# Kernel optimization log

Hardware: AMD Instinct MI355X
Metric: run time of the kernel (lower is better)

## Reference

```python
import jax, jax.numpy as jnp
import numpy as np

N_HEADS = 16
N_EMBD = 1024
HEAD_DIM = N_EMBD // N_HEADS
WINDOW = 512
B, T = 2, 2048


def setup_inputs() -> dict:
    key = jax.random.key(0)
    ks = jax.random.split(key, 5)
    s = 0.02
    return {
        "x": jax.random.normal(ks[0], (B, T, N_EMBD), dtype=jnp.float32),
        "Wq": jax.random.normal(ks[1], (N_EMBD, N_EMBD), dtype=jnp.float32) * s,
        "Wk": jax.random.normal(ks[2], (N_EMBD, N_EMBD), dtype=jnp.float32) * s,
        "Wv": jax.random.normal(ks[3], (N_EMBD, N_EMBD), dtype=jnp.float32) * s,
        "Wo": jax.random.normal(ks[4], (N_EMBD, N_EMBD), dtype=jnp.float32) * s,
    }


def _sliding_window_mask(T, window):
    # mask[i, j] True iff max(0, i-window+1) <= j <= i  (causal banded)
    i = jnp.arange(T)[:, None]
    j = jnp.arange(T)[None, :]
    return (j <= i) & (j > i - window)


def reference(x, Wq, Wk, Wv, Wo):
    Bb, Tt, C = x.shape
    # nn.Linear applies x @ W.T; we store W as [in, out] so just x @ W
    def heads(w):
        return (x @ w).reshape(Bb, Tt, N_HEADS, HEAD_DIM).transpose(0, 2, 1, 3)
    q, k, v = heads(Wq), heads(Wk), heads(Wv)  # [B, H, T, D]
    scores = jnp.einsum("bhqd,bhkd->bhqk", q, k) / jnp.sqrt(jnp.float32(HEAD_DIM))
    mask = _sliding_window_mask(Tt, WINDOW)  # [T, T]
    scores = jnp.where(mask[None, None], scores, jnp.float32(-jnp.inf))
    attn = jax.nn.softmax(scores, axis=-1)
    out = jnp.einsum("bhqk,bhkd->bhqd", attn, v)  # [B, H, T, D]
    out = out.transpose(0, 2, 1, 3).reshape(Bb, Tt, C)
    return out @ Wo
```

## Files before the change

### kernel.cpp

```cpp
#include <hip/hip_runtime.h>

#define B_SZ 2
#define T_SZ 2048
#define C_SZ 1024
#define K_SZ 1024
#define QKV_LD 3072
#define H_CNT 16
#define D_SZ 64
#define WIN 512

typedef __bf16 bf16_t;
typedef bf16_t bf16x8 __attribute__((ext_vector_type(8)));
typedef bf16_t bf16x4 __attribute__((ext_vector_type(4)));
typedef float f32x4 __attribute__((ext_vector_type(4)));
typedef unsigned int u32;

__device__ __forceinline__ f32x4 mfma16(bf16x8 a, bf16x8 b, f32x4 c) {
  return __builtin_amdgcn_mfma_f32_16x16x32_bf16(a, b, c, 0, 0, 0);
}

__device__ __forceinline__ void gload_lds16(const void* gsrc, void* ldst) {
  auto g = (__attribute__((address_space(1))) void*)(unsigned long long)gsrc;
  auto l = (__attribute__((address_space(3))) void*)(unsigned int)(unsigned long long)ldst;
  __builtin_amdgcn_global_load_lds(g, l, 16, 0, 0);
}

__global__ __launch_bounds__(256) void prep(
    const float* __restrict__ x, bf16_t* __restrict__ xb,
    const float* __restrict__ W0, const float* __restrict__ W1,
    const float* __restrict__ W2, const float* __restrict__ W3,
    bf16_t* __restrict__ T0, bf16_t* __restrict__ T1,
    bf16_t* __restrict__ T2, bf16_t* __restrict__ T3) {
  if (blockIdx.z == 4) {
    const int base = (blockIdx.y * 32 + blockIdx.x) * 256 + threadIdx.x;
#pragma unroll
    for (int j = 0; j < 4; ++j) {
      const int idx = base + j * 262144;
      const float4 v = ((const float4*)x)[idx];
      bf16x4 r;
      r[0] = (bf16_t)v.x; r[1] = (bf16_t)v.y; r[2] = (bf16_t)v.z; r[3] = (bf16_t)v.w;
      ((bf16x4*)xb)[idx] = r;
    }
    return;
  }
  __shared__ float tile[32][33];
  const float* W = blockIdx.z == 0 ? W0 : blockIdx.z == 1 ? W1 : blockIdx.z == 2 ? W2 : W3;
  bf16_t* Tt = blockIdx.z == 0 ? T0 : blockIdx.z == 1 ? T1 : blockIdx.z == 2 ? T2 : T3;
  const int tx = threadIdx.x & 31, ty = threadIdx.x >> 5;
  const int r0 = blockIdx.y * 32, c0 = blockIdx.x * 32;
#pragma unroll
  for (int i = 0; i < 4; ++i)
    tile[ty + i * 8][tx] = W[(size_t)(r0 + ty + i * 8) * C_SZ + c0 + tx];
  __syncthreads();
#pragma unroll
  for (int i = 0; i < 4; ++i)
    Tt[(size_t)(c0 + ty + i * 8) * C_SZ + r0 + tx] = (bf16_t)tile[tx][ty + i * 8];
}

#define GM_NT 16

__global__ __launch_bounds__(512, 2) void gemm256(
    const bf16_t* __restrict__ A, const bf16_t* __restrict__ Bt,
    bf16_t* __restrict__ C, bf16_t* __restrict__ Vt) {
  __shared__ __align__(16) bf16_t As[2][256 * 64];
  __shared__ __align__(16) bf16_t Bs[2][192 * 64];
  const int wg = blockIdx.x + 16 * blockIdx.y;
  const int swz = (wg & 7) * 32 + (wg >> 3);
  const int bx = swz & 15, by = swz >> 4;
  const int m0 = by * 256, n0 = bx * 192;
  const int tid = threadIdx.x, w = tid >> 6, lane = tid & 63;
  const int wr = w >> 1, wc = w & 1;
  const int g = lane >> 4, l15 = lane & 15, sw = l15 & 7;
  const int srow = lane >> 3, sj = lane & 7;

  f32x4 acc[4][6] = {};

  auto stageA = [&](int buf, int half, int k0) {
#pragma unroll
    for (int q8 = 0; q8 < 2; ++q8) {
      const int rg = w * 16 + q8 * 8;
      gload_lds16(A + (size_t)(m0 + half * 128 + rg + srow) * K_SZ + k0 + ((sj ^ srow) << 3),
                  &As[buf][half * 8192 + rg * 64]);
    }
  };
  auto stageB = [&](int buf, int third, int k0) {
    const int rg = third * 64 + w * 8;
    gload_lds16(Bt + (size_t)(n0 + rg + srow) * K_SZ + k0 + ((sj ^ srow) << 3),
                &Bs[buf][rg * 64]);
  };

  stageA(0, 0, 0); stageA(0, 1, 0);
  stageB(0, 0, 0); stageB(0, 1, 0); stageB(0, 2, 0);

#define LDAF(MF, KK) \
  (*(const bf16x8*)&As[buf][(wr * 64 + (MF) * 16 + l15) * 64 + \
                            ((((KK) << 2) | g) ^ sw) * 8])
#define LDBF(NF, KK) \
  (*(const bf16x8*)&Bs[buf][(wc * 96 + (NF) * 16 + l15) * 64 + \
                            ((((KK) << 2) | g) ^ sw) * 8])
#define MROW(MF, AF)                              \
  acc[(MF)][0] = mfma16(AF, b0, acc[(MF)][0]);    \
  acc[(MF)][1] = mfma16(AF, b1, acc[(MF)][1]);    \
  acc[(MF)][2] = mfma16(AF, b2, acc[(MF)][2]);    \
  acc[(MF)][3] = mfma16(AF, b3, acc[(MF)][3]);    \
  acc[(MF)][4] = mfma16(AF, b4, acc[(MF)][4]);    \
  acc[(MF)][5] = mfma16(AF, b5, acc[(MF)][5]);

#pragma unroll 2
  for (int t = 0; t < GM_NT; ++t) {
    const int buf = t & 1, nb = buf ^ 1;
    const int k1 = (t + 1) * 64;
    asm volatile("s_waitcnt vmcnt(0)" ::: "memory");
    __builtin_amdgcn_s_barrier();

    {
      bf16x8 a0 = LDAF(0, 0), a1 = LDAF(1, 0), a2 = LDAF(2, 0), a3 = LDAF(3, 0);
      bf16x8 b0 = LDBF(0, 0), b1 = LDBF(1, 0), b2 = LDBF(2, 0),
             b3 = LDBF(3, 0), b4 = LDBF(4, 0), b5 = LDBF(5, 0);
      if (t < GM_NT - 1) { stageA(nb, 0, k1); stageA(nb, 1, k1); }
      __builtin_amdgcn_s_barrier();
      __builtin_amdgcn_s_setprio(1);
      MROW(0, a0) MROW(1, a1) MROW(2, a2) MROW(3, a3)
      __builtin_amdgcn_s_setprio(0);
      __builtin_amdgcn_s_barrier();
    }
    {
      bf16x8 a0 = LDAF(0, 1), a1 = LDAF(1, 1), a2 = LDAF(2, 1), a3 = LDAF(3, 1);
      bf16x8 b0 = LDBF(0, 1), b1 = LDBF(1, 1), b2 = LDBF(2, 1),
             b3 = LDBF(3, 1), b4 = LDBF(4, 1), b5 = LDBF(5, 1);
      if (t < GM_NT - 1) { stageB(nb, 0, k1); stageB(nb, 1, k1); stageB(nb, 2, k1); }
      __builtin_amdgcn_s_barrier();
      __builtin_amdgcn_s_setprio(1);
      MROW(0, a0) MROW(1, a1) MROW(2, a2) MROW(3, a3)
      __builtin_amdgcn_s_setprio(0);
    }
  }

#pragma unroll
  for (int mf = 0; mf < 4; ++mf) {
    const int row = m0 + wr * 64 + mf * 16 + g * 4;
#pragma unroll
    for (int nf = 0; nf < 6; ++nf) {
      const int colb = n0 + wc * 96 + nf * 16;
      if (colb >= 2048) {
        const int d = colb - 2048 + l15;
        const size_t vo =
            ((size_t)((row >> 11) * 16 + (d >> 6)) * 64 + (d & 63)) * (size_t)T_SZ +
            (row & (T_SZ - 1));
        union { bf16_t h4[4]; uint2 u; } pk;
#pragma unroll
        for (int i = 0; i < 4; ++i) pk.h4[i] = (bf16_t)acc[mf][nf][i];
        *(uint2*)(Vt + vo) = pk.u;
      } else {
#pragma unroll
        for (int i = 0; i < 4; ++i)
          C[(size_t)(row + i) * QKV_LD + colb + l15] = (bf16_t)acc[mf][nf][i];
      }
    }
  }
}

__global__ __launch_bounds__(512, 4) void gemm128(
    const bf16_t* __restrict__ A, int lda, const bf16_t* __restrict__ Bt,
    float* __restrict__ C, int N) {
  __shared__ __align__(16) bf16_t As[2][128 * 64];
  __shared__ __align__(16) bf16_t Bs[2][128 * 64];
  const int wg = blockIdx.x + 8 * blockIdx.y;
  const int swz = (wg & 7) * 32 + (wg >> 3);
  const int bx = swz & 7, by = swz >> 3;
  const int m0 = by * 128, n0 = bx * 128;
  const int tid = threadIdx.x, w = tid >> 6, lane = tid & 63;
  const int wr = w >> 2, wc = w & 3;
  const int g = lane >> 4, l15 = lane & 15, sw = l15 & 7;
  const int srow = lane >> 3, sj = lane & 7;

  f32x4 acc[4][2] = {};

  auto stage = [&](int buf, int k0) {
#pragma unroll
    for (int half = 0; half < 2; ++half) {
      const int rg = half * 64 + w * 8;
      gload_lds16(A + (size_t)(m0 + rg + srow) * lda + k0 + ((sj ^ srow) << 3),
                  &As[buf][rg * 64]);
      gload_lds16(Bt + (size_t)(n0 + rg + srow) * K_SZ + k0 + ((sj ^ srow) << 3),
                  &Bs[buf][rg * 64]);
    }
  };

  stage(0, 0);

#pragma unroll 2
  for (int t = 0; t < GM_NT; ++t) {
    const int buf = t & 1;
    asm volatile("s_waitcnt vmcnt(0)" ::: "memory");
    __builtin_amdgcn_s_barrier();
    if (t < GM_NT - 1) stage(buf ^ 1, (t + 1) * 64);
#pragma unroll
    for (int kk = 0; kk < 2; ++kk) {
      bf16x8 af[4], bfr[2];
#pragma unroll
      for (int mf = 0; mf < 4; ++mf)
        af[mf] = *(const bf16x8*)&As[buf][(wr * 64 + mf * 16 + l15) * 64 +
                                          (((kk << 2) | g) ^ sw) * 8];
#pragma unroll
      for (int nf = 0; nf < 2; ++nf)
        bfr[nf] = *(const bf16x8*)&Bs[buf][(wc * 32 + nf * 16 + l15) * 64 +
                                           (((kk << 2) | g) ^ sw) * 8];
      __builtin_amdgcn_s_setprio(1);
#pragma unroll
      for (int mf = 0; mf < 4; ++mf)
#pragma unroll
        for (int nf = 0; nf < 2; ++nf)
          acc[mf][nf] = mfma16(af[mf], bfr[nf], acc[mf][nf]);
      __builtin_amdgcn_s_setprio(0);
    }
  }

#pragma unroll
  for (int mf = 0; mf < 4; ++mf)
#pragma unroll
    for (int nf = 0; nf < 2; ++nf)
#pragma unroll
      for (int i = 0; i < 4; ++i)
        C[(size_t)(m0 + wr * 64 + mf * 16 + g * 4 + i) * N +
          n0 + wc * 32 + nf * 16 + l15] = acc[mf][nf][i];
}

__global__ __launch_bounds__(512) void attn_kernel(
    bf16_t* __restrict__ QKV, const bf16_t* __restrict__ Vt) {
  __shared__ __align__(16) bf16_t Kl[2][64 * 64];
  __shared__ __align__(16) bf16_t Vl[2][64 * 64];

  const int qt = ((blockIdx.x & 7) << 1) | (blockIdx.x >> 3);
  const int bh = blockIdx.y;
  const int b = bh >> 4, h = bh & 15;
  const int q0 = qt * 128;
  const int tid = threadIdx.x, w = tid >> 6, lane = tid & 63;
  const int g = lane >> 4, l15 = lane & 15, gh = g >> 1;
  const int wrow0 = q0 + w * 16;
  const int myrow = wrow0 + l15;
  const int sub = lane >> 3, jj = lane & 7;
  const int sw = l15 & 7;

  auto stage = [&](int bufi, int kt) {
    const int row = w * 8 + sub;
    const int sj = jj ^ sub;
    gload_lds16(QKV + ((size_t)b * T_SZ + kt + row) * QKV_LD + 1024 + h * D_SZ + sj * 8,
                &Kl[bufi][w * 512]);
    gload_lds16(Vt + ((size_t)bh * D_SZ + row) * T_SZ + kt + sj * 8,
                &Vl[bufi][w * 512]);
  };

  bf16x8 qf[2];
  {
    const bf16_t* qptr = QKV + ((size_t)b * T_SZ + myrow) * QKV_LD + h * D_SZ;
    const float QSC = 0.125f * 1.44269504f;
#pragma unroll
    for (int c2 = 0; c2 < 2; ++c2) {
      bf16x8 t = *(const bf16x8*)(qptr + c2 * 32 + g * 8);
      bf16x8 o;
#pragma unroll
      for (int j = 0; j < 8; ++j) o[j] = (bf16_t)((float)t[j] * QSC);
      qf[c2] = o;
    }
  }

  float m_s = -1e30f, l_s = 0.f;
  f32x4 oacc[4] = {};

  int kstart = q0 - (WIN - 1);
  if (kstart < 0) kstart = 0;
  kstart &= ~63;
  const int nt = (q0 + 128 - kstart) >> 6;

  stage(0, kstart);

  for (int it = 0; it < nt; ++it) {
    const int kt = kstart + (it << 6);
    const int cur = it & 1;
    if (it + 1 < nt) {
      stage(cur ^ 1, kt + 64);
      asm volatile("s_waitcnt vmcnt(2)" ::: "memory");
    } else {
      asm volatile("s_waitcnt vmcnt(0)" ::: "memory");
    }
    __builtin_amdgcn_s_barrier();
    __builtin_amdgcn_sched_barrier(0);

    const bool skip = (kt + 63 < wrow0 - (WIN - 1)) || (kt > wrow0 + 15);
    if (!skip) {
      f32x4 s[4] = {};
#pragma unroll
      for (int t = 0; t < 4; ++t) {
        const bf16_t* kbase = &Kl[cur][(t * 16 + l15) * 64];
#pragma unroll
        for (int c2 = 0; c2 < 2; ++c2) {
          const bf16x8 kf = *(const bf16x8*)(kbase + (((c2 * 4 + g) ^ sw) << 3));
          s[t] = mfma16(kf, qf[c2], s[t]);
        }
      }

      const bool interior = (kt + 63 <= wrow0) && (kt >= wrow0 + 15 - (WIN - 1));
      float sv[4][4];
      if (interior) {
#pragma unroll
        for (int t = 0; t < 4; ++t)
#pragma unroll
          for (int i = 0; i < 4; ++i) sv[t][i] = s[t][i];
      } else {
#pragma unroll
        for (int t = 0; t < 4; ++t)
#pragma unroll
          for (int i = 0; i < 4; ++i) {
            const int kk = kt + t * 16 + g * 4 + i;
            sv[t][i] = (kk <= myrow && kk > myrow - WIN) ? s[t][i] : -1e30f;
          }
      }

      float mx = sv[0][0];
#pragma unroll
      for (int t = 0; t < 4; ++t)
#pragma unroll
        for (int i = 0; i < 4; ++i)
          if (t || i) mx = fmaxf(mx, sv[t][i]);
      mx = fmaxf(mx, __shfl_xor(mx, 16));
      mx = fmaxf(mx, __shfl_xor(mx, 32));

      float mbase;
      const bool defer = __all((mx <= m_s + 8.f) && (m_s > -1e29f));
      if (defer) {
        mbase = m_s;
      } else {
        const float mnew = fmaxf(m_s, mx);
        const float scl = exp2f(m_s - mnew);
        m_s = mnew;
        mbase = (mnew > -1e29f) ? mnew : 1e30f;
        float sc4[4];
#pragma unroll
        for (int i = 0; i < 4; ++i) sc4[i] = __shfl(scl, g * 4 + i, 16);
#pragma unroll
        for (int c = 0; c < 4; ++c)
#pragma unroll
          for (int i = 0; i < 4; ++i) oacc[c][i] *= sc4[i];
        l_s *= scl;
      }

      float p[4][4];
      float rsum = 0.f;
#pragma unroll
      for (int t = 0; t < 4; ++t)
#pragma unroll
        for (int i = 0; i < 4; ++i) {
          p[t][i] = exp2f(sv[t][i] - mbase);
          rsum += p[t][i];
        }
      rsum += __shfl_xor(rsum, 16);
      rsum += __shfl_xor(rsum, 32);
      l_s += rsum;

      u32 Wp[4][2];
#pragma unroll
      for (int t = 0; t < 4; ++t)
#pragma unroll
        for (int w2 = 0; w2 < 2; ++w2) {
          union { bf16_t hh[2]; u32 uu; } pk;
          pk.hh[0] = (bf16_t)p[t][2 * w2];
          pk.hh[1] = (bf16_t)p[t][2 * w2 + 1];
          Wp[t][w2] = pk.uu;
        }

#pragma unroll
      for (int kp = 0; kp < 2; ++kp) {
        const u32 lo0 = Wp[2 * kp][0], lo1 = Wp[2 * kp][1];
        const u32 hi0 = Wp[2 * kp + 1][0], hi1 = Wp[2 * kp + 1][1];
        union { u32 u[4]; bf16x8 v; } pa;
        pa.u[0] = gh ? hi0 : lo0;
        pa.u[1] = gh ? hi1 : lo1;
        pa.u[2] = (u32)__shfl_xor((int)(gh ? lo0 : hi0), 32);
        pa.u[3] = (u32)__shfl_xor((int)(gh ? lo1 : hi1), 32);

        const int tA = 2 * kp + gh;
        const int low = (g & 1) * 4;
        const int cA = ((tA * 2 + gh) ^ sw) << 3;
        const int cB = ((tA * 2 + (gh ^ 1)) ^ sw) << 3;
#pragma unroll
        for (int c = 0; c < 4; ++c) {
          const bf16_t* vbase = &Vl[cur][(c * 16 + l15) * 64];
          union { bf16x4 h[2]; bf16x8 v; } vv;
          vv.h[0] = *(const bf16x4*)(vbase + cA + low);
          vv.h[1] = *(const bf16x4*)(vbase + cB + low);
          oacc[c] = mfma16(pa.v, vv.v, oacc[c]);
        }
      }
    }
    __builtin_amdgcn_sched_barrier(0);
    __builtin_amdgcn_s_barrier();
  }

  const float invl = 1.0f / l_s;
  float inv4[4];
#pragma unroll
  for (int i = 0; i < 4; ++i) inv4[i] = __shfl(invl, g * 4 + i, 16);
#pragma unroll
  for (int i = 0; i < 4; ++i) {
    const size_t ro = ((size_t)b * T_SZ + wrow0 + g * 4 + i) * QKV_LD + 2048 + h * D_SZ;
#pragma unroll
    for (int c = 0; c < 4; ++c)
      QKV[ro + c * 16 + l15] = (bf16_t)(oacc[c][i] * inv4[i]);
  }
}

extern "C" void kernel_launch(void* const* d_in, const int* in_sizes, int n_in,
                              void* d_out, int out_size, void* d_ws, size_t ws_size,
                              hipStream_t stream) {
  const float* x = (const float*)d_in[0];
  const float* Wq = (const float*)d_in[1];
  const float* Wk = (const float*)d_in[2];
  const float* Wv = (const float*)d_in[3];
  const float* Wo = (const float*)d_in[4];
  float* out = (float*)d_out;
  char* ws = (char*)d_ws;
  const size_t MB = 1ull << 20;
  bf16_t* xb = (bf16_t*)(ws);
  bf16_t* QKVb = (bf16_t*)(ws + 8 * MB);
  bf16_t* WqT = (bf16_t*)(ws + 32 * MB);
  bf16_t* WkT = (bf16_t*)(ws + 34 * MB);
  bf16_t* WvT = (bf16_t*)(ws + 36 * MB);
  bf16_t* WoT = (bf16_t*)(ws + 38 * MB);
  bf16_t* Vtp = (bf16_t*)(ws + 48 * MB);

  prep<<<dim3(32, 32, 5), 256, 0, stream>>>(x, xb, Wq, Wk, Wv, Wo,
                                            WqT, WkT, WvT, WoT);
  gemm256<<<dim3(16, 16), 512, 0, stream>>>(xb, WqT, QKVb, Vtp);
  attn_kernel<<<dim3(16, B_SZ * H_CNT), 512, 0, stream>>>(QKVb, Vtp);
  gemm128<<<dim3(8, 32), 512, 0, stream>>>(QKVb + 2048, QKV_LD, WoT, out, C_SZ);
}
```

Measured before the change: 86.11 us.

## Fuse fp32-to-bf16 input conversion into QKV GEMM and retile output GEMM

Removes the separate x-to-bf16 pass from the prep kernel. The QKV GEMM now loads fp32 x directly into registers, converts it to bf16, and writes the swizzled tile into LDS itself, which avoids writing and re-reading an intermediate bf16 copy of x. In exchange, A-tile staging uses register round-trips instead of direct global-to-LDS loads and reads twice the bytes for A. Separately, the output projection GEMM is retiled to 128x64 tiles with 256 threads and twice as many workgroups, with an extra barrier per k-step.

```diff
diff --git a/kernel.cpp b/kernel.cpp
--- a/kernel.cpp
+++ b/kernel.cpp
@@ -13,6 +13,7 @@
 typedef bf16_t bf16x8 __attribute__((ext_vector_type(8)));
 typedef bf16_t bf16x4 __attribute__((ext_vector_type(4)));
 typedef float f32x4 __attribute__((ext_vector_type(4)));
+typedef float f32x4v __attribute__((ext_vector_type(4)));
 typedef unsigned int u32;
 
 __device__ __forceinline__ f32x4 mfma16(bf16x8 a, bf16x8 b, f32x4 c) {
@@ -26,23 +27,10 @@
 }
 
 __global__ __launch_bounds__(256) void prep(
-    const float* __restrict__ x, bf16_t* __restrict__ xb,
     const float* __restrict__ W0, const float* __restrict__ W1,
     const float* __restrict__ W2, const float* __restrict__ W3,
     bf16_t* __restrict__ T0, bf16_t* __restrict__ T1,
     bf16_t* __restrict__ T2, bf16_t* __restrict__ T3) {
-  if (blockIdx.z == 4) {
-    const int base = (blockIdx.y * 32 + blockIdx.x) * 256 + threadIdx.x;
-#pragma unroll
-    for (int j = 0; j < 4; ++j) {
-      const int idx = base + j * 262144;
-      const float4 v = ((const float4*)x)[idx];
-      bf16x4 r;
-      r[0] = (bf16_t)v.x; r[1] = (bf16_t)v.y; r[2] = (bf16_t)v.z; r[3] = (bf16_t)v.w;
-      ((bf16x4*)xb)[idx] = r;
-    }
-    return;
-  }
   __shared__ float tile[32][33];
   const float* W = blockIdx.z == 0 ? W0 : blockIdx.z == 1 ? W1 : blockIdx.z == 2 ? W2 : W3;
   bf16_t* Tt = blockIdx.z == 0 ? T0 : blockIdx.z == 1 ? T1 : blockIdx.z == 2 ? T2 : T3;
@@ -60,7 +48,7 @@
 #define GM_NT 16
 
 __global__ __launch_bounds__(512, 2) void gemm256(
-    const bf16_t* __restrict__ A, const bf16_t* __restrict__ Bt,
+    const float* __restrict__ X, const bf16_t* __restrict__ Bt,
     bf16_t* __restrict__ C, bf16_t* __restrict__ Vt) {
   __shared__ __align__(16) bf16_t As[2][256 * 64];
   __shared__ __align__(16) bf16_t Bs[2][192 * 64];
@@ -74,13 +62,30 @@
   const int srow = lane >> 3, sj = lane & 7;
 
   f32x4 acc[4][6] = {};
-
-  auto stageA = [&](int buf, int half, int k0) {
-#pragma unroll
-    for (int q8 = 0; q8 < 2; ++q8) {
+  f32x4v areg[8];
+
+  auto loadA = [&](int k0) {
+#pragma unroll
+    for (int u = 0; u < 4; ++u) {
+      const int half = u >> 1, q8 = u & 1;
+      const int row = m0 + half * 128 + w * 16 + q8 * 8 + srow;
+      const float* p = X + (size_t)row * K_SZ + k0 + ((sj ^ srow) << 3);
+      areg[2 * u] = *(const f32x4v*)p;
+      areg[2 * u + 1] = *(const f32x4v*)(p + 4);
+    }
+  };
+  auto writeA = [&](int buf) {
+#pragma unroll
+    for (int u = 0; u < 4; ++u) {
+      const int half = u >> 1, q8 = u & 1;
       const int rg = w * 16 + q8 * 8;
-      gload_lds16(A + (size_t)(m0 + half * 128 + rg + srow) * K_SZ + k0 + ((sj ^ srow) << 3),
-                  &As[buf][half * 8192 + rg * 64]);
+      bf16x8 o;
+#pragma unroll
+      for (int j = 0; j < 4; ++j) {
+        o[j] = (bf16_t)areg[2 * u][j];
+        o[4 + j] = (bf16_t)areg[2 * u + 1][j];
+      }
+      *(bf16x8*)&As[buf][half * 8192 + rg * 64 + srow * 64 + sj * 8] = o;
     }
   };
   auto stageB = [&](int buf, int third, int k0) {
@@ -89,8 +94,10 @@
                 &Bs[buf][rg * 64]);
   };
 
-  stageA(0, 0, 0); stageA(0, 1, 0);
+  loadA(0);
   stageB(0, 0, 0); stageB(0, 1, 0); stageB(0, 2, 0);
+  asm volatile("s_waitcnt vmcnt(3)" ::: "memory");
+  writeA(0);
 
 #define LDAF(MF, KK) \
   (*(const bf16x8*)&As[buf][(wr * 64 + (MF) * 16 + l15) * 64 + \
@@ -110,14 +117,14 @@
   for (int t = 0; t < GM_NT; ++t) {
     const int buf = t & 1, nb = buf ^ 1;
     const int k1 = (t + 1) * 64;
-    asm volatile("s_waitcnt vmcnt(0)" ::: "memory");
+    asm volatile("s_waitcnt vmcnt(0) lgkmcnt(0)" ::: "memory");
     __builtin_amdgcn_s_barrier();
 
     {
       bf16x8 a0 = LDAF(0, 0), a1 = LDAF(1, 0), a2 = LDAF(2, 0), a3 = LDAF(3, 0);
       bf16x8 b0 = LDBF(0, 0), b1 = LDBF(1, 0), b2 = LDBF(2, 0),
              b3 = LDBF(3, 0), b4 = LDBF(4, 0), b5 = LDBF(5, 0);
-      if (t < GM_NT - 1) { stageA(nb, 0, k1); stageA(nb, 1, k1); }
+      if (t < GM_NT - 1) loadA(k1);
       __builtin_amdgcn_s_barrier();
       __builtin_amdgcn_s_setprio(1);
       MROW(0, a0) MROW(1, a1) MROW(2, a2) MROW(3, a3)
@@ -128,7 +135,11 @@
       bf16x8 a0 = LDAF(0, 1), a1 = LDAF(1, 1), a2 = LDAF(2, 1), a3 = LDAF(3, 1);
       bf16x8 b0 = LDBF(0, 1), b1 = LDBF(1, 1), b2 = LDBF(2, 1),
              b3 = LDBF(3, 1), b4 = LDBF(4, 1), b5 = LDBF(5, 1);
-      if (t < GM_NT - 1) { stageB(nb, 0, k1); stageB(nb, 1, k1); stageB(nb, 2, k1); }
+      if (t < GM_NT - 1) {
+        stageB(nb, 0, k1); stageB(nb, 1, k1); stageB(nb, 2, k1);
+        asm volatile("s_waitcnt vmcnt(3)" ::: "memory");
+        writeA(nb);
+      }
       __builtin_amdgcn_s_barrier();
       __builtin_amdgcn_s_setprio(1);
       MROW(0, a0) MROW(1, a1) MROW(2, a2) MROW(3, a3)
@@ -160,17 +171,17 @@
   }
 }
 
-__global__ __launch_bounds__(512, 4) void gemm128(
+__global__ __launch_bounds__(256, 3) void gemm128(
     const bf16_t* __restrict__ A, int lda, const bf16_t* __restrict__ Bt,
     float* __restrict__ C, int N) {
   __shared__ __align__(16) bf16_t As[2][128 * 64];
-  __shared__ __align__(16) bf16_t Bs[2][128 * 64];
-  const int wg = blockIdx.x + 8 * blockIdx.y;
-  const int swz = (wg & 7) * 32 + (wg >> 3);
-  const int bx = swz & 7, by = swz >> 3;
-  const int m0 = by * 128, n0 = bx * 128;
+  __shared__ __align__(16) bf16_t Bs[2][64 * 64];
+  const int wg = blockIdx.x + 16 * blockIdx.y;
+  const int swz = (wg & 7) * 64 + (wg >> 3);
+  const int bx = swz & 15, by = swz >> 4;
+  const int m0 = by * 128, n0 = bx * 64;
   const int tid = threadIdx.x, w = tid >> 6, lane = tid & 63;
-  const int wr = w >> 2, wc = w & 3;
+  const int wr = w >> 1, wc = w & 1;
   const int g = lane >> 4, l15 = lane & 15, sw = l15 & 7;
   const int srow = lane >> 3, sj = lane & 7;
 
@@ -178,10 +189,14 @@
 
   auto stage = [&](int buf, int k0) {
 #pragma unroll
-    for (int half = 0; half < 2; ++half) {
-      const int rg = half * 64 + w * 8;
+    for (int r = 0; r < 4; ++r) {
+      const int rg = (w * 4 + r) * 8;
       gload_lds16(A + (size_t)(m0 + rg + srow) * lda + k0 + ((sj ^ srow) << 3),
                   &As[buf][rg * 64]);
+    }
+#pragma unroll
+    for (int r = 0; r < 2; ++r) {
+      const int rg = (w * 2 + r) * 8;
       gload_lds16(Bt + (size_t)(n0 + rg + srow) * K_SZ + k0 + ((sj ^ srow) << 3),
                   &Bs[buf][rg * 64]);
     }
@@ -214,6 +229,7 @@
           acc[mf][nf] = mfma16(af[mf], bfr[nf], acc[mf][nf]);
       __builtin_amdgcn_s_setprio(0);
     }
+    __builtin_amdgcn_s_barrier();
   }
 
 #pragma unroll
@@ -421,7 +437,6 @@
   float* out = (float*)d_out;
   char* ws = (char*)d_ws;
   const size_t MB = 1ull << 20;
-  bf16_t* xb = (bf16_t*)(ws);
   bf16_t* QKVb = (bf16_t*)(ws + 8 * MB);
   bf16_t* WqT = (bf16_t*)(ws + 32 * MB);
   bf16_t* WkT = (bf16_t*)(ws + 34 * MB);
@@ -429,9 +444,8 @@
   bf16_t* WoT = (bf16_t*)(ws + 38 * MB);
   bf16_t* Vtp = (bf16_t*)(ws + 48 * MB);
 
-  prep<<<dim3(32, 32, 5), 256, 0, stream>>>(x, xb, Wq, Wk, Wv, Wo,
-                                            WqT, WkT, WvT, WoT);
-  gemm256<<<dim3(16, 16), 512, 0, stream>>>(xb, WqT, QKVb, Vtp);
+  prep<<<dim3(32, 32, 4), 256, 0, stream>>>(Wq, Wk, Wv, Wo, WqT, WkT, WvT, WoT);
+  gemm256<<<dim3(16, 16), 512, 0, stream>>>(x, WqT, QKVb, Vtp);
   attn_kernel<<<dim3(16, B_SZ * H_CNT), 512, 0, stream>>>(QKVb, Vtp);
-  gemm128<<<dim3(8, 32), 512, 0, stream>>>(QKVb + 2048, QKV_LD, WoT, out, C_SZ);
-}
+  gemm128<<<dim3(16, 32), 256, 0, stream>>>(QKVb + 2048, QKV_LD, WoT, out, C_SZ);
+}
```

Result: slower. 95.11 us (+10.4%).
